# Performance work log

Measured on AMD Instinct MI355X. Metric: run time of the kernel, lower is better.

## Reference

```python
import jax, jax.numpy as jnp
import numpy as np

EPS = 1e-8  # matches torch F.cosine_similarity eps


def _normalize(x):
    n = jnp.sqrt(jnp.sum(x * x, axis=-1, keepdims=True))
    return x / jnp.maximum(n, EPS)


def _cross_entropy_diag(logits):
    # targets = arange(B): CE = mean(-log_softmax(logits)[i, i])
    logp = jax.nn.log_softmax(logits, axis=-1)
    return -jnp.mean(jnp.diagonal(logp))


def setup_inputs() -> dict:
    key = jax.random.key(0)
    k1, k2, k3 = jax.random.split(key, 3)
    B, D = 8192, 256
    return {
        "heavy_feat": jax.random.normal(k1, (B, D), dtype=jnp.float32),
        "light_feat": jax.random.normal(k2, (B, D), dtype=jnp.float32),
        "antigen_feat": jax.random.normal(k3, (B, D), dtype=jnp.float32),
    }


def reference(heavy_feat, light_feat, antigen_feat):
    h = _normalize(heavy_feat)   # [B, D]
    l = _normalize(light_feat)   # [B, D]
    a = _normalize(antigen_feat)  # [B, D]
    ha_sim = jnp.einsum("id,jd->ij", h, a)  # [B, B] cosine sims
    hl_sim = jnp.einsum("id,jd->ij", l, a)  # [B, B]
    return _cross_entropy_diag(ha_sim) + _cross_entropy_diag(hl_sim)
```

## Files before the change

kernel.cpp:

```cpp
#include <hip/hip_runtime.h>
#include <stdint.h>

#define BN_ 8192
#define DK_ 256
#define LOG2E 1.4426950408889634f
#define INVQ (1.0f / 16129.0f)
#define KQ   (LOG2E / 16129.0f)

typedef __attribute__((ext_vector_type(4))) float f32x4;
typedef __attribute__((ext_vector_type(4))) int i32x4;

#define GLD16(gp, lp)                                                   \
  __builtin_amdgcn_global_load_lds(                                     \
      (__attribute__((address_space(1))) void*)(gp),                    \
      (__attribute__((address_space(3))) void*)(lp), 16, 0, 0)

#define BAR() __builtin_amdgcn_s_barrier()
#define VM4() asm volatile("s_waitcnt vmcnt(4)" ::: "memory")
#define VM0() asm volatile("s_waitcnt vmcnt(0)" ::: "memory")

__global__ __launch_bounds__(256) void norm_kernel(
    const float* __restrict__ hf, const float* __restrict__ lf,
    const float* __restrict__ af, unsigned char* __restrict__ qbase,
    float* __restrict__ sumexp) {
  const int tid = threadIdx.x;
  if (blockIdx.x < 16) {
    f32x4 z = {0.f, 0.f, 0.f, 0.f};
    *(f32x4*)(sumexp + blockIdx.x * 1024 + tid * 4) = z;
  }
  const int w = tid >> 6, lane = tid & 63;
  const int grow = blockIdx.x * 4 + w;
  const int m = grow >> 13;
  const int r = grow & (BN_ - 1);
  const float* src = (m == 0) ? hf : (m == 1) ? lf : af;
  unsigned char* dst = qbase + (size_t)m * BN_ * DK_;
  const float4 v = ((const float4*)(src + (size_t)r * DK_))[lane];
  float ss = v.x * v.x + v.y * v.y + v.z * v.z + v.w * v.w;
#pragma unroll
  for (int mk = 32; mk >= 1; mk >>= 1) ss += __shfl_xor(ss, mk, 64);
  const float inv = 127.0f / fmaxf(sqrtf(ss), 1e-8f);
  const int q0 = (int)rintf(v.x * inv), q1 = (int)rintf(v.y * inv);
  const int q2 = (int)rintf(v.z * inv), q3 = (int)rintf(v.w * inv);
  const unsigned pk = (q0 & 255) | ((q1 & 255) << 8) | ((q2 & 255) << 16) |
                      ((unsigned)(q3 & 255) << 24);
  *(unsigned*)(dst + (size_t)r * DK_ + lane * 4) = pk;
}

__global__ __launch_bounds__(512, 2) void gemm_lse_kernel(
    const unsigned char* __restrict__ hl, const unsigned char* __restrict__ an,
    float* __restrict__ sumexp , float* __restrict__ diag ) {
  extern __shared__ char lds[];

  const int tid = threadIdx.x;
  const int lane = tid & 63, w = tid >> 6;
  const int wr = w >> 2, wc = w & 3;
  const int lmod = lane & 15, lhalf = lane >> 4;

  const int bid = blockIdx.x;
  const int swz = (bid & 7) * 32 + (bid >> 3);
  const int mt = swz >> 1;
  const int cg = swz & 1;

  const int aswz = 16 * ((tid & 15) ^ ((tid >> 4) & 15));
  const unsigned char* aG = hl + (size_t)(mt * 128 + (tid >> 4)) * DK_ + aswz;
  char* aD = lds + tid * 16;
  GLD16(aG, aD);
  GLD16(aG + 8192, aD + 8192);
  GLD16(aG + 16384, aD + 16384);
  GLD16(aG + 24576, aD + 24576);

  const int slog16 = 16 * ((lane & 3) ^ ((lane >> 3) & 3));
  const unsigned char* bB =
      an + (size_t)(cg * 4096 + wc * 64 + (lane >> 2)) * DK_ + slog16;
  char* ldsB = lds + 32768 + w * 8192 + lane * 16;

#define STAGEB(uu)                                                       \
  do {                                                                   \
    const int ct_ = (uu) >> 2, ku_ = (uu) & 3;                           \
    const unsigned char* g_ = bB + ct_ * 65536 + ku_ * 64;               \
    char* d_ = ldsB + ((uu) & 1) * 4096;                                 \
    GLD16(g_, d_);                                                       \
    GLD16(g_ + 4096, d_ + 1024);                                         \
    GLD16(g_ + 8192, d_ + 2048);                                         \
    GLD16(g_ + 12288, d_ + 3072);                                        \
  } while (0)

  STAGEB(0);
  VM4();
  BAR();

  i32x4 afr[4][4];
  {
    const char* aR = lds + (wr * 64 + lmod) * 256;
#pragma unroll
    for (int ku = 0; ku < 4; ++ku)
#pragma unroll
      for (int m = 0; m < 4; ++m)
        afr[ku][m] = *(const i32x4*)(aR + m * 4096 + 16 * ((ku * 4 + lhalf) ^ lmod));
  }

  const int rdoffB = lmod * 64 + 16 * (lhalf ^ ((lmod >> 1) & 3));
  const char* ldsBr = lds + 32768 + w * 8192;

  const int p = mt >> 6;
  const int D = (mt & 63) * 128 + wr * 64;
  const bool dWave = (wc == ((D >> 6) & 3)) && ((D >> 12) == cg);
  const int ctD = (D >> 8) & 15;

  float rsum[4][4];
#pragma unroll
  for (int m = 0; m < 4; ++m)
#pragma unroll
    for (int r = 0; r < 4; ++r) rsum[m][r] = 0.0f;

#pragma unroll 1
  for (int ct = 0; ct < 16; ++ct) {
    i32x4 acc[4][4];
#pragma unroll
    for (int m = 0; m < 4; ++m)
#pragma unroll
      for (int n = 0; n < 4; ++n) acc[m][n] = i32x4{0, 0, 0, 0};

#pragma unroll
    for (int ku = 0; ku < 4; ++ku) {
      const int u = ct * 4 + ku;
      if (u < 63) {
        STAGEB(u + 1);
        VM4();
      } else {
        VM0();
      }
      const char* Lb = ldsBr + (ku & 1) * 4096;
      i32x4 bf[4];
#pragma unroll
      for (int n = 0; n < 4; ++n) bf[n] = *(const i32x4*)(Lb + n * 1024 + rdoffB);
      __builtin_amdgcn_s_setprio(1);
#pragma unroll
      for (int m = 0; m < 4; ++m)
#pragma unroll
        for (int n = 0; n < 4; ++n)
          acc[m][n] = __builtin_amdgcn_mfma_i32_16x16x64_i8(afr[ku][m], bf[n], acc[m][n], 0, 0, 0);
      __builtin_amdgcn_s_setprio(0);
    }

    if (dWave && ct == ctD) {
#pragma unroll
      for (int m = 0; m < 4; ++m)
#pragma unroll
        for (int r = 0; r < 4; ++r)
          if (lmod == lhalf * 4 + r)
            diag[p * BN_ + D + m * 16 + lmod] = (float)acc[m][m][r] * INVQ;
    }
#pragma unroll
    for (int m = 0; m < 4; ++m)
#pragma unroll
      for (int n = 0; n < 4; ++n)
#pragma unroll
        for (int r = 0; r < 4; ++r)
          rsum[m][r] += __builtin_amdgcn_exp2f((float)acc[m][n][r] * KQ);
  }

#pragma unroll
  for (int m = 0; m < 4; ++m)
#pragma unroll
    for (int r = 0; r < 4; ++r) {
      float v = rsum[m][r];
      v += __shfl_xor(v, 1, 64);
      v += __shfl_xor(v, 2, 64);
      v += __shfl_xor(v, 4, 64);
      v += __shfl_xor(v, 8, 64);
      if (lmod == 0)
        atomicAdd(&sumexp[p * BN_ + D + m * 16 + lhalf * 4 + r], v);
    }
#undef STAGEB
}

__global__ __launch_bounds__(1024) void finalize_kernel(
    const float* __restrict__ sumexp, const float* __restrict__ diag,
    float* __restrict__ out) {
  const int tid = threadIdx.x;
  float s = 0.0f;
  for (int i = tid; i < 2 * BN_; i += 1024) s += logf(sumexp[i]) - diag[i];
#pragma unroll
  for (int mk = 32; mk >= 1; mk >>= 1) s += __shfl_xor(s, mk, 64);
  __shared__ float red[16];
  if ((tid & 63) == 0) red[tid >> 6] = s;
  __syncthreads();
  if (tid == 0) {
    float t = 0.f;
#pragma unroll
    for (int j = 0; j < 16; ++j) t += red[j];
    out[0] = t * (1.0f / (float)BN_);
  }
}

extern "C" void kernel_launch(void* const* d_in, const int* in_sizes, int n_in,
                              void* d_out, int out_size, void* d_ws, size_t ws_size,
                              hipStream_t stream) {
  const float* hf = (const float*)d_in[0];
  const float* lf = (const float*)d_in[1];
  const float* af = (const float*)d_in[2];

  char* ws = (char*)d_ws;
  const size_t nmat = (size_t)BN_ * DK_;
  unsigned char* qbase = (unsigned char*)ws;
  unsigned char* hl = qbase;
  unsigned char* an = qbase + 2 * nmat;
  float* sumexp = (float*)(ws + 3 * nmat);
  float* diag = sumexp + 2 * BN_;

  hipFuncSetAttribute((const void*)gemm_lse_kernel,
                      hipFuncAttributeMaxDynamicSharedMemorySize, 98304);

  norm_kernel<<<(3 * BN_) / 4, 256, 0, stream>>>(hf, lf, af, qbase, sumexp);
  gemm_lse_kernel<<<256, 512, 98304, stream>>>(hl, an, sumexp, diag);
  finalize_kernel<<<1, 1024, 0, stream>>>(sumexp, diag, (float*)d_out);
}
```

Baseline: 63.95 us.

## Triple-buffer B tiles in LDS and prefetch next B fragments into registers

Each wave's private B staging area goes from a double buffer to a rotating triple buffer, so two global-to-LDS loads are in flight instead of one. The next step's B fragments are also read from LDS into registers before the current 16 MFMAs run, so LDS read latency overlaps with matrix work. The aim is to hide global-load and LDS latency in the int8 GEMM loop. The cost is 32KB more dynamic LDS (128KB per block), extra registers for the second fragment set, and a more complex hand-unrolled schedule with a special-cased tail.

```diff
diff --git a/kernel.cpp b/kernel.cpp
--- a/kernel.cpp
+++ b/kernel.cpp
@@ -72,20 +72,24 @@
   const int slog16 = 16 * ((lane & 3) ^ ((lane >> 3) & 3));
   const unsigned char* bB =
       an + (size_t)(cg * 4096 + wc * 64 + (lane >> 2)) * DK_ + slog16;
-  char* ldsB = lds + 32768 + w * 8192 + lane * 16;
-
-#define STAGEB(uu)                                                       \
+  char* bw = lds + 32768 + w * 12288;
+  char* c0 = bw;
+  char* c1 = bw + 4096;
+  char* c2 = bw + 8192;
+
+#define STAGEB(uu, DST)                                                  \
   do {                                                                   \
     const int ct_ = (uu) >> 2, ku_ = (uu) & 3;                           \
     const unsigned char* g_ = bB + ct_ * 65536 + ku_ * 64;               \
-    char* d_ = ldsB + ((uu) & 1) * 4096;                                 \
+    char* d_ = (DST) + lane * 16;                                        \
     GLD16(g_, d_);                                                       \
     GLD16(g_ + 4096, d_ + 1024);                                         \
     GLD16(g_ + 8192, d_ + 2048);                                         \
     GLD16(g_ + 12288, d_ + 3072);                                        \
   } while (0)
 
-  STAGEB(0);
+  STAGEB(0, c0);
+  STAGEB(1, c1);
   VM4();
   BAR();
 
@@ -100,7 +104,26 @@
   }
 
   const int rdoffB = lmod * 64 + 16 * (lhalf ^ ((lmod >> 1) & 3));
-  const char* ldsBr = lds + 32768 + w * 8192;
+
+  i32x4 bfc[4], bfn[4];
+#pragma unroll
+  for (int n = 0; n < 4; ++n)
+    bfc[n] = *(const i32x4*)(c0 + n * 1024 + rdoffB);
+
+#define RDNXT(SRC)                                                       \
+  _Pragma("unroll") for (int n = 0; n < 4; ++n)                          \
+      bfn[n] = *(const i32x4*)((SRC) + n * 1024 + rdoffB)
+
+#define CPB()                                                            \
+  _Pragma("unroll") for (int n = 0; n < 4; ++n) bfc[n] = bfn[n]
+
+#define MFMA16(KU)                                                       \
+  __builtin_amdgcn_s_setprio(1);                                         \
+  _Pragma("unroll") for (int m = 0; m < 4; ++m)                          \
+  _Pragma("unroll") for (int n = 0; n < 4; ++n)                          \
+      acc[m][n] = __builtin_amdgcn_mfma_i32_16x16x64_i8(                 \
+          afr[KU][m], bfc[n], acc[m][n], 0, 0, 0);                       \
+  __builtin_amdgcn_s_setprio(0)
 
   const int p = mt >> 6;
   const int D = (mt & 63) * 128 + wr * 64;
@@ -121,26 +144,17 @@
 #pragma unroll
       for (int n = 0; n < 4; ++n) acc[m][n] = i32x4{0, 0, 0, 0};
 
-#pragma unroll
-    for (int ku = 0; ku < 4; ++ku) {
-      const int u = ct * 4 + ku;
-      if (u < 63) {
-        STAGEB(u + 1);
-        VM4();
-      } else {
-        VM0();
-      }
-      const char* Lb = ldsBr + (ku & 1) * 4096;
-      i32x4 bf[4];
-#pragma unroll
-      for (int n = 0; n < 4; ++n) bf[n] = *(const i32x4*)(Lb + n * 1024 + rdoffB);
-      __builtin_amdgcn_s_setprio(1);
-#pragma unroll
-      for (int m = 0; m < 4; ++m)
-#pragma unroll
-        for (int n = 0; n < 4; ++n)
-          acc[m][n] = __builtin_amdgcn_mfma_i32_16x16x64_i8(afr[ku][m], bf[n], acc[m][n], 0, 0, 0);
-      __builtin_amdgcn_s_setprio(0);
+    const int u0 = ct * 4;
+    if (ct < 15) {
+      STAGEB(u0 + 2, c2); VM4(); RDNXT(c1); MFMA16(0); CPB();
+      STAGEB(u0 + 3, c0); VM4(); RDNXT(c2); MFMA16(1); CPB();
+      STAGEB(u0 + 4, c1); VM4(); RDNXT(c0); MFMA16(2); CPB();
+      STAGEB(u0 + 5, c2); VM4(); RDNXT(c1); MFMA16(3); CPB();
+    } else {
+      STAGEB(62, c2); VM4(); RDNXT(c1); MFMA16(0); CPB();
+      STAGEB(63, c0); VM4(); RDNXT(c2); MFMA16(1); CPB();
+      VM0();           RDNXT(c0); MFMA16(2); CPB();
+      MFMA16(3);
     }
 
     if (dWave && ct == ctD) {
@@ -158,6 +172,8 @@
 #pragma unroll
         for (int r = 0; r < 4; ++r)
           rsum[m][r] += __builtin_amdgcn_exp2f((float)acc[m][n][r] * KQ);
+
+    char* t = c0; c0 = c1; c1 = c2; c2 = t;
   }
 
 #pragma unroll
@@ -173,6 +189,9 @@
         atomicAdd(&sumexp[p * BN_ + D + m * 16 + lhalf * 4 + r], v);
     }
 #undef STAGEB
+#undef RDNXT
+#undef CPB
+#undef MFMA16
 }
 
 __global__ __launch_bounds__(1024) void finalize_kernel(
@@ -210,9 +229,9 @@
   float* diag = sumexp + 2 * BN_;
 
   hipFuncSetAttribute((const void*)gemm_lse_kernel,
-                      hipFuncAttributeMaxDynamicSharedMemorySize, 98304);
+                      hipFuncAttributeMaxDynamicSharedMemorySize, 131072);
 
   norm_kernel<<<(3 * BN_) / 4, 256, 0, stream>>>(hf, lf, af, qbase, sumexp);
-  gemm_lse_kernel<<<256, 512, 98304, stream>>>(hl, an, sumexp, diag);
+  gemm_lse_kernel<<<256, 512, 131072, stream>>>(hl, an, sumexp, diag);
   finalize_kernel<<<1, 1024, 0, stream>>>(sumexp, diag, (float*)d_out);
 }
```

After: 66.75 us. 1.04x slower.

## Split GEMM-LSE into 1024 smaller 4-wave blocks over column quarters

Applied to the files above, without the earlier changes.

The fused int8 GEMM plus logsumexp kernel now uses 256-thread blocks covering 64 rows and a quarter of the columns, launched as 1024 blocks instead of 256 blocks of 512 threads. LDS per block halves, so more blocks can be resident per CU and the grid fills 256 CUs more evenly. The s_setprio hints around the MFMA sequence are also removed. In exchange, each A tile is reloaded by more blocks, the sumexp atomics double, and per-block pipeline prologue overhead grows.

```diff
diff --git a/kernel.cpp b/kernel.cpp
--- a/kernel.cpp
+++ b/kernel.cpp
@@ -46,33 +46,32 @@
   *(unsigned*)(dst + (size_t)r * DK_ + lane * 4) = pk;
 }
 
-__global__ __launch_bounds__(512, 2) void gemm_lse_kernel(
+__global__ __launch_bounds__(256, 2) void gemm_lse_kernel(
     const unsigned char* __restrict__ hl, const unsigned char* __restrict__ an,
     float* __restrict__ sumexp , float* __restrict__ diag ) {
   extern __shared__ char lds[];
 
   const int tid = threadIdx.x;
   const int lane = tid & 63, w = tid >> 6;
-  const int wr = w >> 2, wc = w & 3;
   const int lmod = lane & 15, lhalf = lane >> 4;
 
   const int bid = blockIdx.x;
-  const int swz = (bid & 7) * 32 + (bid >> 3);
-  const int mt = swz >> 1;
-  const int cg = swz & 1;
+  const int swz = (bid & 7) * 128 + (bid >> 3);
+  const int mt = swz >> 2;
+  const int cq = swz & 3;
 
   const int aswz = 16 * ((tid & 15) ^ ((tid >> 4) & 15));
-  const unsigned char* aG = hl + (size_t)(mt * 128 + (tid >> 4)) * DK_ + aswz;
+  const unsigned char* aG = hl + (size_t)(mt * 64 + (tid >> 4)) * DK_ + aswz;
   char* aD = lds + tid * 16;
   GLD16(aG, aD);
+  GLD16(aG + 4096, aD + 4096);
   GLD16(aG + 8192, aD + 8192);
-  GLD16(aG + 16384, aD + 16384);
-  GLD16(aG + 24576, aD + 24576);
+  GLD16(aG + 12288, aD + 12288);
 
   const int slog16 = 16 * ((lane & 3) ^ ((lane >> 3) & 3));
   const unsigned char* bB =
-      an + (size_t)(cg * 4096 + wc * 64 + (lane >> 2)) * DK_ + slog16;
-  char* ldsB = lds + 32768 + w * 8192 + lane * 16;
+      an + (size_t)(cq * 2048 + w * 64 + (lane >> 2)) * DK_ + slog16;
+  char* ldsB = lds + 16384 + w * 8192 + lane * 16;
 
 #define STAGEB(uu)                                                       \
   do {                                                                   \
@@ -91,7 +90,7 @@
 
   i32x4 afr[4][4];
   {
-    const char* aR = lds + (wr * 64 + lmod) * 256;
+    const char* aR = lds + lmod * 256;
 #pragma unroll
     for (int ku = 0; ku < 4; ++ku)
 #pragma unroll
@@ -100,12 +99,18 @@
   }
 
   const int rdoffB = lmod * 64 + 16 * (lhalf ^ ((lmod >> 1) & 3));
-  const char* ldsBr = lds + 32768 + w * 8192;
-
-  const int p = mt >> 6;
-  const int D = (mt & 63) * 128 + wr * 64;
-  const bool dWave = (wc == ((D >> 6) & 3)) && ((D >> 12) == cg);
-  const int ctD = (D >> 8) & 15;
+  const char* ldsBr = lds + 16384 + w * 8192;
+
+#define MFMA16(KU)                                                       \
+  _Pragma("unroll") for (int m = 0; m < 4; ++m)                          \
+  _Pragma("unroll") for (int n = 0; n < 4; ++n)                          \
+      acc[m][n] = __builtin_amdgcn_mfma_i32_16x16x64_i8(                 \
+          afr[KU][m], bf[n], acc[m][n], 0, 0, 0)
+
+  const int p = mt >> 7;
+  const int C0 = (mt & 127) * 64;
+  const bool dWave = (cq == (C0 >> 11)) && (w == ((C0 >> 6) & 3));
+  const int ctD = (C0 & 2047) >> 8;
 
   float rsum[4][4];
 #pragma unroll
@@ -114,7 +119,7 @@
     for (int r = 0; r < 4; ++r) rsum[m][r] = 0.0f;
 
 #pragma unroll 1
-  for (int ct = 0; ct < 16; ++ct) {
+  for (int ct = 0; ct < 8; ++ct) {
     i32x4 acc[4][4];
 #pragma unroll
     for (int m = 0; m < 4; ++m)
@@ -124,23 +129,17 @@
 #pragma unroll
     for (int ku = 0; ku < 4; ++ku) {
       const int u = ct * 4 + ku;
-      if (u < 63) {
+      if (u < 31) {
         STAGEB(u + 1);
         VM4();
       } else {
         VM0();
       }
-      const char* Lb = ldsBr + (ku & 1) * 4096;
+      const char* Lb = ldsBr + (u & 1) * 4096;
       i32x4 bf[4];
 #pragma unroll
       for (int n = 0; n < 4; ++n) bf[n] = *(const i32x4*)(Lb + n * 1024 + rdoffB);
-      __builtin_amdgcn_s_setprio(1);
-#pragma unroll
-      for (int m = 0; m < 4; ++m)
-#pragma unroll
-        for (int n = 0; n < 4; ++n)
-          acc[m][n] = __builtin_amdgcn_mfma_i32_16x16x64_i8(afr[ku][m], bf[n], acc[m][n], 0, 0, 0);
-      __builtin_amdgcn_s_setprio(0);
+      MFMA16(ku);
     }
 
     if (dWave && ct == ctD) {
@@ -149,7 +148,7 @@
 #pragma unroll
         for (int r = 0; r < 4; ++r)
           if (lmod == lhalf * 4 + r)
-            diag[p * BN_ + D + m * 16 + lmod] = (float)acc[m][m][r] * INVQ;
+            diag[p * BN_ + C0 + m * 16 + lmod] = (float)acc[m][m][r] * INVQ;
     }
 #pragma unroll
     for (int m = 0; m < 4; ++m)
@@ -170,9 +169,10 @@
       v += __shfl_xor(v, 4, 64);
       v += __shfl_xor(v, 8, 64);
       if (lmod == 0)
-        atomicAdd(&sumexp[p * BN_ + D + m * 16 + lhalf * 4 + r], v);
+        atomicAdd(&sumexp[p * BN_ + C0 + m * 16 + lhalf * 4 + r], v);
     }
 #undef STAGEB
+#undef MFMA16
 }
 
 __global__ __launch_bounds__(1024) void finalize_kernel(
@@ -210,9 +210,9 @@
   float* diag = sumexp + 2 * BN_;
 
   hipFuncSetAttribute((const void*)gemm_lse_kernel,
-                      hipFuncAttributeMaxDynamicSharedMemorySize, 98304);
+                      hipFuncAttributeMaxDynamicSharedMemorySize, 49152);
 
   norm_kernel<<<(3 * BN_) / 4, 256, 0, stream>>>(hf, lf, af, qbase, sumexp);
-  gemm_lse_kernel<<<256, 512, 98304, stream>>>(hl, an, sumexp, diag);
+  gemm_lse_kernel<<<1024, 256, 49152, stream>>>(hl, an, sumexp, diag);
   finalize_kernel<<<1, 1024, 0, stream>>>(sumexp, diag, (float*)d_out);
 }
```

Result: slower. 66.73 us (+4.3%).

## Double-buffer accumulators to overlap exp epilogue with next tile's MFMAs

Applied to the files above, without the earlier changes.

The accumulator tile is now ping-ponged between two register sets, so the exp2/row-sum epilogue of the previous column tile is interleaved, one row chunk at a time, with the MFMA loop of the current tile. The point is to hide the transcendental epilogue behind matrix-core work. To make room for the second accumulator set, the A fragments are no longer kept in registers for the whole kernel and are re-read from LDS at every k-step. The setprio hints are also dropped. The cost is extra LDS traffic and higher register pressure, which could lead to spills.

```diff
diff --git a/kernel.cpp b/kernel.cpp
--- a/kernel.cpp
+++ b/kernel.cpp
@@ -89,16 +89,7 @@
   VM4();
   BAR();
 
-  i32x4 afr[4][4];
-  {
-    const char* aR = lds + (wr * 64 + lmod) * 256;
-#pragma unroll
-    for (int ku = 0; ku < 4; ++ku)
-#pragma unroll
-      for (int m = 0; m < 4; ++m)
-        afr[ku][m] = *(const i32x4*)(aR + m * 4096 + 16 * ((ku * 4 + lhalf) ^ lmod));
-  }
-
+  const char* aR = lds + (wr * 64 + lmod) * 256;
   const int rdoffB = lmod * 64 + 16 * (lhalf ^ ((lmod >> 1) & 3));
   const char* ldsBr = lds + 32768 + w * 8192;
 
@@ -113,52 +104,59 @@
 #pragma unroll
     for (int r = 0; r < 4; ++r) rsum[m][r] = 0.0f;
 
+  i32x4 accA[4][4], accB[4][4];
+
+#define EPCHUNK(OTH, M, PCT)                                             \
+  do {                                                                   \
+    if (dWave && (PCT) == ctD) {                                         \
+      _Pragma("unroll") for (int r = 0; r < 4; ++r)                      \
+          if (lmod == lhalf * 4 + r)                                     \
+            diag[p * BN_ + D + (M) * 16 + lmod] =                        \
+                (float)OTH[M][M][r] * INVQ;                              \
+    }                                                                    \
+    _Pragma("unroll") for (int n = 0; n < 4; ++n)                        \
+    _Pragma("unroll") for (int r = 0; r < 4; ++r)                        \
+        rsum[M][r] += __builtin_amdgcn_exp2f((float)OTH[M][n][r] * KQ);  \
+  } while (0)
+
+#define CTBODY(ACC, OTH, CT, DOEP)                                       \
+  do {                                                                   \
+    _Pragma("unroll") for (int m = 0; m < 4; ++m)                        \
+    _Pragma("unroll") for (int n = 0; n < 4; ++n)                        \
+        ACC[m][n] = i32x4{0, 0, 0, 0};                                   \
+    _Pragma("unroll") for (int ku = 0; ku < 4; ++ku) {                   \
+      const int u = (CT) * 4 + ku;                                       \
+      if (u < 63) {                                                      \
+        STAGEB(u + 1);                                                   \
+        VM4();                                                           \
+      } else {                                                           \
+        VM0();                                                           \
+      }                                                                  \
+      const char* Lb = ldsBr + (u & 1) * 4096;                           \
+      i32x4 af[4], bf[4];                                                \
+      _Pragma("unroll") for (int n = 0; n < 4; ++n)                      \
+          bf[n] = *(const i32x4*)(Lb + n * 1024 + rdoffB);               \
+      _Pragma("unroll") for (int m = 0; m < 4; ++m)                      \
+          af[m] = *(const i32x4*)(aR + m * 4096 +                        \
+                                  16 * ((ku * 4 + lhalf) ^ lmod));       \
+      _Pragma("unroll") for (int m = 0; m < 4; ++m)                      \
+      _Pragma("unroll") for (int n = 0; n < 4; ++n)                      \
+          ACC[m][n] = __builtin_amdgcn_mfma_i32_16x16x64_i8(             \
+              af[m], bf[n], ACC[m][n], 0, 0, 0);                         \
+      if (DOEP) EPCHUNK(OTH, ku, (CT)-1);                                \
+    }                                                                    \
+  } while (0)
+
+  CTBODY(accA, accB, 0, 0);
 #pragma unroll 1
-  for (int ct = 0; ct < 16; ++ct) {
-    i32x4 acc[4][4];
-#pragma unroll
-    for (int m = 0; m < 4; ++m)
-#pragma unroll
-      for (int n = 0; n < 4; ++n) acc[m][n] = i32x4{0, 0, 0, 0};
-
-#pragma unroll
-    for (int ku = 0; ku < 4; ++ku) {
-      const int u = ct * 4 + ku;
-      if (u < 63) {
-        STAGEB(u + 1);
-        VM4();
-      } else {
-        VM0();
-      }
-      const char* Lb = ldsBr + (ku & 1) * 4096;
-      i32x4 bf[4];
-#pragma unroll
-      for (int n = 0; n < 4; ++n) bf[n] = *(const i32x4*)(Lb + n * 1024 + rdoffB);
-      __builtin_amdgcn_s_setprio(1);
-#pragma unroll
-      for (int m = 0; m < 4; ++m)
-#pragma unroll
-        for (int n = 0; n < 4; ++n)
-          acc[m][n] = __builtin_amdgcn_mfma_i32_16x16x64_i8(afr[ku][m], bf[n], acc[m][n], 0, 0, 0);
-      __builtin_amdgcn_s_setprio(0);
-    }
-
-    if (dWave && ct == ctD) {
-#pragma unroll
-      for (int m = 0; m < 4; ++m)
-#pragma unroll
-        for (int r = 0; r < 4; ++r)
-          if (lmod == lhalf * 4 + r)
-            diag[p * BN_ + D + m * 16 + lmod] = (float)acc[m][m][r] * INVQ;
-    }
-#pragma unroll
-    for (int m = 0; m < 4; ++m)
-#pragma unroll
-      for (int n = 0; n < 4; ++n)
-#pragma unroll
-        for (int r = 0; r < 4; ++r)
-          rsum[m][r] += __builtin_amdgcn_exp2f((float)acc[m][n][r] * KQ);
+  for (int cp = 0; cp < 7; ++cp) {
+    const int c1 = cp * 2 + 1;
+    CTBODY(accB, accA, c1, 1);
+    CTBODY(accA, accB, c1 + 1, 1);
   }
+  CTBODY(accB, accA, 15, 1);
+#pragma unroll
+  for (int m = 0; m < 4; ++m) EPCHUNK(accB, m, 15);
 
 #pragma unroll
   for (int m = 0; m < 4; ++m)
@@ -173,6 +171,8 @@
         atomicAdd(&sumexp[p * BN_ + D + m * 16 + lhalf * 4 + r], v);
     }
 #undef STAGEB
+#undef EPCHUNK
+#undef CTBODY
 }
 
 __global__ __launch_bounds__(1024) void finalize_kernel(
```

Result: slower. 77.04 us (+20.5%).
